# Performance work log

Hardware: AMD Instinct MI355X
Metric: run time of the kernel (lower is better)

The kernel has to match this reference:

```python
import jax, jax.numpy as jnp
import numpy as np

N_NODES = 100000


def _gcn_layer(x, W, b, src, dst, n):
    # PyG GCNConv: x' = D^-1/2 (A+I) D^-1/2 (x W) + b, with self-loops added.
    x = x @ W  # [N, out]
    loop = jnp.arange(n, dtype=src.dtype)
    src_f = jnp.concatenate([src, loop])
    dst_f = jnp.concatenate([dst, loop])
    deg = jax.ops.segment_sum(jnp.ones_like(dst_f, dtype=x.dtype), dst_f, num_segments=n)
    dinv = jnp.where(deg > 0, jax.lax.rsqrt(deg), 0.0)
    norm = dinv[src_f] * dinv[dst_f]  # [E+N]
    msgs = x[src_f] * norm[:, None]   # gather + scale
    out = jax.ops.segment_sum(msgs, dst_f, num_segments=n)
    return out + b


def setup_inputs() -> dict:
    key = jax.random.key(0)
    ks = jax.random.split(key, 16)
    inputFeatures = jax.random.normal(ks[0], (N_NODES, 64), dtype=jnp.float32)
    edge_index = jax.random.randint(ks[1], (2, 1000000), 0, N_NODES, dtype=jnp.int64)

    def lin(k, fan_in, fan_out):
        s = 1.0 / np.sqrt(fan_in)
        return jax.random.uniform(k, (fan_in, fan_out), jnp.float32, -s, s)

    return {
        "inputFeatures": inputFeatures,
        "W1": lin(ks[2], 64, 100), "b1": jnp.zeros((100,), jnp.float32),
        "W2": lin(ks[3], 100, 50), "b2": jnp.zeros((50,), jnp.float32),
        "W3": lin(ks[4], 50, 25), "b3": jnp.zeros((25,), jnp.float32),
        "Wl1": lin(ks[5], 25, 25), "bl1": jnp.zeros((25,), jnp.float32),
        "Wl2": lin(ks[6], 25, 10), "bl2": jnp.zeros((10,), jnp.float32),
        "Wl3": lin(ks[7], 10, 1), "bl3": jnp.zeros((1,), jnp.float32),
        "edge_index": edge_index,
    }


def reference(inputFeatures, W1, b1, W2, b2, W3, b3, Wl1, bl1, Wl2, bl2, Wl3, bl3, edge_index):
    src, dst = edge_index[0], edge_index[1]
    n = inputFeatures.shape[0]
    x = jax.nn.relu(_gcn_layer(inputFeatures, W1, b1, src, dst, n))
    x = jax.nn.relu(_gcn_layer(x, W2, b2, src, dst, n))
    x = jax.nn.relu(_gcn_layer(x, W3, b3, src, dst, n))
    x = jax.nn.relu(x @ Wl1 + bl1)
    x = jax.nn.relu(x @ Wl2 + bl2)
    x = jax.nn.relu(x @ Wl3 + bl3)
    return x  # [N, 1]
```

## Files before the change

### kernel.cpp

```cpp
#include <hip/hip_runtime.h>
#include <hip/hip_fp16.h>
#include <cstdint>

constexpr int BSHIFT = 9;
constexpr int NBUCK  = 256;
constexpr int BUCKET_CAP = 6144;
constexpr int BN = 1 << BSHIFT;
constexpr int NT = 8;

struct alignas(16) H8 { __half2 a, b, c, d; };
struct alignas(8)  H4 { __half2 a, b; };

typedef _Float16 f16x8 __attribute__((ext_vector_type(8)));
typedef float    f32x4 __attribute__((ext_vector_type(4)));

__device__ __forceinline__ float4 add4(float4 a, float4 b) {
    return make_float4(a.x + b.x, a.y + b.y, a.z + b.z, a.w + b.w);
}
__device__ __forceinline__ float4 mul4s(float4 a, float s) {
    return make_float4(a.x * s, a.y * s, a.z * s, a.w * s);
}
__device__ __forceinline__ void acc_h8(float4& A0, float4& A1, const H8 v, float s) {
    float2 f0 = __half22float2(v.a), f1 = __half22float2(v.b);
    float2 f2 = __half22float2(v.c), f3 = __half22float2(v.d);
    A0.x = fmaf(f0.x, s, A0.x); A0.y = fmaf(f0.y, s, A0.y);
    A0.z = fmaf(f1.x, s, A0.z); A0.w = fmaf(f1.y, s, A0.w);
    A1.x = fmaf(f2.x, s, A1.x); A1.y = fmaf(f2.y, s, A1.y);
    A1.z = fmaf(f3.x, s, A1.z); A1.w = fmaf(f3.y, s, A1.w);
}


constexpr int EPT = 16;
__global__ __launch_bounds__(256) void partition_pack(
    const int* __restrict__ src, const int* __restrict__ dst,
    int* __restrict__ bucketCur, int* __restrict__ pairs, int ne, int nEdgeBlocks,
    const float* __restrict__ W1, const float* __restrict__ W2,
    const float* __restrict__ W3,
    __half* __restrict__ P1, __half* __restrict__ P2, __half* __restrict__ P3) {
    if (blockIdx.x == (unsigned)nEdgeBlocks) {
        int t = threadIdx.x;
        for (int i = t; i < 7 * 2 * 64 * 8; i += 256) {
            int j = i & 7, lane = (i >> 3) & 63, f = i >> 9;
            int mt = f >> 1, kf = f & 1;
            int k = kf * 32 + (lane >> 4) * 8 + j;
            int m = mt * 16 + (lane & 15);
            P1[i] = __float2half_rn(m < 100 ? W1[k * 100 + m] : 0.0f);
        }
        for (int i = t; i < 4 * 4 * 64 * 8; i += 256) {
            int j = i & 7, lane = (i >> 3) & 63, f = i >> 9;
            int mt = f >> 2, kf = f & 3;
            int k = kf * 32 + (lane >> 4) * 8 + j;
            int m = mt * 16 + (lane & 15);
            P2[i] = __float2half_rn((k < 100 && m < 50) ? W2[k * 50 + m] : 0.0f);
        }
        for (int i = t; i < 2 * 2 * 64 * 8; i += 256) {
            int j = i & 7, lane = (i >> 3) & 63, f = i >> 9;
            int mt = f >> 1, kf = f & 1;
            int k = kf * 32 + (lane >> 4) * 8 + j;
            int m = mt * 16 + (lane & 15);
            P3[i] = __float2half_rn((k < 50 && m < 25) ? W3[k * 25 + m] : 0.0f);
        }
        return;
    }
    __shared__ int lcnt[NBUCK];
    __shared__ int lbase[NBUCK];
    int base = blockIdx.x * (256 * EPT);
    if (threadIdx.x < NBUCK) lcnt[threadIdx.x] = 0;
    __syncthreads();
    int2 ed[EPT];
    int  rnk[EPT];
#pragma unroll
    for (int j = 0; j < EPT; ++j) {
        int e = base + j * 256 + threadIdx.x;
        if (e < ne) {
            int d = dst[e];
            ed[j] = make_int2(src[e], d);
            rnk[j] = atomicAdd(&lcnt[d >> BSHIFT], 1);
        } else {
            ed[j].y = -1;
        }
    }
    __syncthreads();
    if (threadIdx.x < NBUCK) {
        int c = lcnt[threadIdx.x];
        lbase[threadIdx.x] = c ? atomicAdd(&bucketCur[threadIdx.x], c) : 0;
    }
    __syncthreads();
#pragma unroll
    for (int j = 0; j < EPT; ++j) {
        if (ed[j].y >= 0) {
            int b = ed[j].y >> BSHIFT;
            int p = lbase[b] + rnk[j];
            if (p < BUCKET_CAP)
                pairs[(size_t)b * BUCKET_CAP + p] =
                    (ed[j].x << BSHIFT) | (ed[j].y & (BN - 1));
        }
    }
}

__global__ __launch_bounds__(256) void bucket_csr_scan(
    const int* __restrict__ pairs, const int* __restrict__ bucketCnt,
    int* __restrict__ offs, float* __restrict__ dinv, int* __restrict__ csr,
    int n, int ne, int nbuckets) {
    __shared__ int pos2[BN * NT];
    __shared__ int tmp[256];
    __shared__ int baseS;
    int b = blockIdx.x;
    int t = threadIdx.x;

    int c = (t < (unsigned)nbuckets) ? bucketCnt[t] : 0;
    tmp[t] = c;
    for (int i = t; i < BN * NT; i += 256) pos2[i] = 0;
    __syncthreads();
    for (int off = 1; off < 256; off <<= 1) {
        int v = (t >= (unsigned)off) ? tmp[t - off] : 0;
        __syncthreads();
        tmp[t] += v;
        __syncthreads();
    }
    if (t == 0) {
        baseS = b ? tmp[b - 1] : 0;
        if (b == 0) offs[n] = ne;
    }
    __syncthreads();
    int base = baseS;
    int cnt  = bucketCnt[b];
    const int* pb = pairs + (size_t)b * BUCKET_CAP;
    int nodeLo = b << BSHIFT;

    for (int e = t; e < cnt; e += 256) {
        int p = pb[e];
        atomicAdd(&pos2[(p & (BN - 1)) * NT + (((unsigned)p) >> (BSHIFT + 14))], 1);
    }
    __syncthreads();

    {
        int lo = t * 16;
        int s = 0;
#pragma unroll
        for (int i = 0; i < 16; ++i) { int v = pos2[lo + i]; pos2[lo + i] = s; s += v; }
        tmp[t] = s;
        __syncthreads();
        for (int off = 1; off < 256; off <<= 1) {
            int v = (t >= (unsigned)off) ? tmp[t - off] : 0;
            __syncthreads();
            tmp[t] += v;
            __syncthreads();
        }
        int add = t ? tmp[t - 1] : 0;
#pragma unroll
        for (int i = 0; i < 16; ++i) pos2[lo + i] += add;
    }
    __syncthreads();

    int l0 = 2 * t, l1 = l0 + 1;
    int s0 = pos2[l0 * NT];
    int s1 = pos2[l1 * NT];
    int s2 = (t < 255) ? pos2[(l1 + 1) * NT] : cnt;
    int h0 = s1 - s0, h1 = s2 - s1;
    int g0 = nodeLo + l0, g1 = nodeLo + l1;
    if (g0 < n) { offs[g0] = base + s0; dinv[g0] = rsqrtf((float)(h0 + 1)); }
    if (g1 < n) { offs[g1] = base + s1; dinv[g1] = rsqrtf((float)(h1 + 1)); }
    __syncthreads();

    for (int e = t; e < cnt; e += 256) {
        int p = pb[e];
        int idx = (p & (BN - 1)) * NT + (((unsigned)p) >> (BSHIFT + 14));
        int pos = atomicAdd(&pos2[idx], 1);
        csr[base + pos] = ((unsigned)p) >> BSHIFT;
    }
}

__global__ void cvt_scale_f32_f16(const float* __restrict__ x, const float* __restrict__ dinv,
                                  __half* __restrict__ o, int n4) {
    int i = blockIdx.x * blockDim.x + threadIdx.x;
    if (i < n4) {
        float dv = dinv[i >> 4];
        float4 v = ((const float4*)x)[i];
        H4 h;
        h.a = __floats2half2_rn(v.x * dv, v.y * dv);
        h.b = __floats2half2_rn(v.z * dv, v.w * dv);
        ((H4*)o)[i] = h;
    }
}

constexpr int XSP = 72;
constexpr int HPS = 136;
__global__ __launch_bounds__(256, 4) void agg1gemm12(
    const __half* __restrict__ x, const int* __restrict__ offs,
    const int* __restrict__ csr, const float* __restrict__ dinv,
    const __half* __restrict__ P1, const float* __restrict__ b1,
    const __half* __restrict__ P2, __half* __restrict__ out, int n) {
    __shared__ alignas(16) _Float16 Xs[64 * XSP];
    __shared__ alignas(16) _Float16 Hs[64 * HPS];
    int tid = threadIdx.x, lane = tid & 63, w = tid >> 6;
    int lg = lane >> 4, lr = lane & 15;
    int blockBase = blockIdx.x * 64;

    for (int i = tid; i < 64 * 2; i += 256) {
        f16x8 zz = {};
        *(f16x8*)&Hs[(i >> 1) * HPS + 112 + (i & 1) * 8] = zz;
    }

    int f0 = (lane & 7) * 8;
#pragma unroll
    for (int p = 0; p < 2; ++p) {
        int nl = w * 16 + p * 8 + (lane >> 3);
        int node = blockBase + nl;
        float4 z4 = make_float4(0.f, 0.f, 0.f, 0.f);
        float4 a00 = z4, a01 = z4, a10 = z4, a11 = z4, a20 = z4, a21 = z4, a30 = z4, a31 = z4;
        float dv = 0.0f;
        if (node < n) {
            dv = dinv[node];
            H8 sv = *(const H8*)&x[(size_t)node * 64 + f0];
            acc_h8(a00, a01, sv, 1.0f);
            int e0 = offs[node], e1 = offs[node + 1];
            int e = e0;
            for (; e + 4 <= e1; e += 4) {
                int i0 = csr[e], i1 = csr[e + 1], i2 = csr[e + 2], i3 = csr[e + 3];
                H8 v0 = *(const H8*)&x[(size_t)i0 * 64 + f0];
                H8 v1 = *(const H8*)&x[(size_t)i1 * 64 + f0];
                H8 v2 = *(const H8*)&x[(size_t)i2 * 64 + f0];
                H8 v3 = *(const H8*)&x[(size_t)i3 * 64 + f0];
                acc_h8(a00, a01, v0, 1.0f);
                acc_h8(a10, a11, v1, 1.0f);
                acc_h8(a20, a21, v2, 1.0f);
                acc_h8(a30, a31, v3, 1.0f);
            }
            for (; e < e1; ++e) {
                H8 v = *(const H8*)&x[(size_t)csr[e] * 64 + f0];
                acc_h8(a00, a01, v, 1.0f);
            }
        }
        float4 A0 = add4(add4(a00, a10), add4(a20, a30));
        float4 A1 = add4(add4(a01, a11), add4(a21, a31));
        A0 = mul4s(A0, dv);
        A1 = mul4s(A1, dv);
        H8 h;
        h.a = __floats2half2_rn(A0.x, A0.y);
        h.b = __floats2half2_rn(A0.z, A0.w);
        h.c = __floats2half2_rn(A1.x, A1.y);
        h.d = __floats2half2_rn(A1.z, A1.w);
        *(H8*)&Xs[nl * XSP + f0] = h;
    }
    __syncthreads();

    const f16x8* P1v = (const f16x8*)P1;
    float b1v[7];
#pragma unroll
    for (int mt = 0; mt < 7; ++mt) {
        int m = mt * 16 + lr;
        b1v[mt] = (m < 100) ? b1[m] : 0.0f;
    }
    {
        int rowL = w * 16 + lr;
        f16x8 a0 = *(const f16x8*)&Xs[rowL * XSP + lg * 8];
        f16x8 a1 = *(const f16x8*)&Xs[rowL * XSP + 32 + lg * 8];
        int hbase = w * 16;
#pragma unroll
        for (int mt = 0; mt < 7; ++mt) {
            f16x8 w0 = P1v[(mt * 2 + 0) * 64 + lane];
            f16x8 w1 = P1v[(mt * 2 + 1) * 64 + lane];
            f32x4 acc = {};
            acc = __builtin_amdgcn_mfma_f32_16x16x32_f16(a0, w0, acc, 0, 0, 0);
            acc = __builtin_amdgcn_mfma_f32_16x16x32_f16(a1, w1, acc, 0, 0, 0);
            int col = mt * 16 + lr;
#pragma unroll
            for (int i = 0; i < 4; ++i) {
                int rloc = hbase + lg * 4 + i;
                Hs[rloc * HPS + col] = (_Float16)fmaxf(acc[i] + b1v[mt], 0.0f);
            }
        }
    }
    __syncthreads();

    const f16x8* P2v = (const f16x8*)P2;
#pragma unroll
    for (int mt = 0; mt < 4; ++mt) {
        f16x8 w0 = P2v[(mt * 4 + 0) * 64 + lane];
        f16x8 w1 = P2v[(mt * 4 + 1) * 64 + lane];
        f16x8 w2 = P2v[(mt * 4 + 2) * 64 + lane];
        f16x8 w3 = P2v[(mt * 4 + 3) * 64 + lane];
        int lbase = w * 16;
        const _Float16* hrow = &Hs[(size_t)(lbase + lr) * HPS];
        f16x8 a0 = *(const f16x8*)&hrow[lg * 8];
        f16x8 a1 = *(const f16x8*)&hrow[32 + lg * 8];
        f16x8 a2 = *(const f16x8*)&hrow[64 + lg * 8];
        f16x8 a3 = *(const f16x8*)&hrow[96 + lg * 8];
        f32x4 acc = {};
        acc = __builtin_amdgcn_mfma_f32_16x16x32_f16(a0, w0, acc, 0, 0, 0);
        acc = __builtin_amdgcn_mfma_f32_16x16x32_f16(a1, w1, acc, 0, 0, 0);
        acc = __builtin_amdgcn_mfma_f32_16x16x32_f16(a2, w2, acc, 0, 0, 0);
        acc = __builtin_amdgcn_mfma_f32_16x16x32_f16(a3, w3, acc, 0, 0, 0);
        int col = mt * 16 + lr;
#pragma unroll
        for (int i = 0; i < 4; ++i) {
            int node = blockBase + lbase + lg * 4 + i;
            if (node < n)
                out[(size_t)node * 64 + col] = __float2half_rn(acc[i] * dinv[node]);
        }
    }
}

constexpr int YP = 72;
__global__ __launch_bounds__(256) void agg2g3(
    const __half* __restrict__ s, const int* __restrict__ offs,
    const int* __restrict__ csr, const float* __restrict__ dinv,
    const float* __restrict__ b2, const __half* __restrict__ P3,
    __half* __restrict__ out, int n) {
    __shared__ alignas(16) _Float16 Ys[32 * YP];
    int tid = threadIdx.x, lane = tid & 63, w = tid >> 6;
    int lg = lane >> 4, lr = lane & 15;
    int blockBase = blockIdx.x * 32;

    int nodeL = tid >> 3;
    int f0 = (tid & 7) * 8;
    int node = blockBase + nodeL;
    float v[8] = {0.f, 0.f, 0.f, 0.f, 0.f, 0.f, 0.f, 0.f};
    if (node < n && f0 < 56) {
        float dv = dinv[node];
        float4 z4 = make_float4(0.f, 0.f, 0.f, 0.f);
        float4 a00 = z4, a01 = z4, a10 = z4, a11 = z4, a20 = z4, a21 = z4, a30 = z4, a31 = z4;
        {
            H8 sv = *(const H8*)&s[(size_t)node * 64 + f0];
            acc_h8(a00, a01, sv, 1.0f);
        }
        int e0 = offs[node], e1 = offs[node + 1];
        int e = e0;
        for (; e + 4 <= e1; e += 4) {
            int i0 = csr[e], i1 = csr[e + 1], i2 = csr[e + 2], i3 = csr[e + 3];
            H8 v0 = *(const H8*)&s[(size_t)i0 * 64 + f0];
            H8 v1 = *(const H8*)&s[(size_t)i1 * 64 + f0];
            H8 v2 = *(const H8*)&s[(size_t)i2 * 64 + f0];
            H8 v3 = *(const H8*)&s[(size_t)i3 * 64 + f0];
            acc_h8(a00, a01, v0, 1.0f);
            acc_h8(a10, a11, v1, 1.0f);
            acc_h8(a20, a21, v2, 1.0f);
            acc_h8(a30, a31, v3, 1.0f);
        }
        for (; e < e1; ++e) {
            H8 vv = *(const H8*)&s[(size_t)csr[e] * 64 + f0];
            acc_h8(a00, a01, vv, 1.0f);
        }
        float4 A0 = add4(add4(a00, a10), add4(a20, a30));
        float4 A1 = add4(add4(a01, a11), add4(a21, a31));
        float vr[8] = {A0.x, A0.y, A0.z, A0.w, A1.x, A1.y, A1.z, A1.w};
#pragma unroll
        for (int i = 0; i < 8; ++i)
            v[i] = (f0 + i < 50) ? fmaxf(dv * vr[i] + b2[f0 + i], 0.0f) : 0.0f;
    }
    {
        H8 h;
        h.a = __floats2half2_rn(v[0], v[1]);
        h.b = __floats2half2_rn(v[2], v[3]);
        h.c = __floats2half2_rn(v[4], v[5]);
        h.d = __floats2half2_rn(v[6], v[7]);
        *(H8*)&Ys[nodeL * YP + f0] = h;
    }
    __syncthreads();

    int rt = w >> 1, mt = w & 1;
    const f16x8* P3v = (const f16x8*)P3;
    f16x8 w0 = P3v[(mt * 2 + 0) * 64 + lane];
    f16x8 w1 = P3v[(mt * 2 + 1) * 64 + lane];
    int rowL = rt * 16 + lr;
    f16x8 a0 = *(const f16x8*)&Ys[rowL * YP + lg * 8];
    f16x8 a1 = *(const f16x8*)&Ys[rowL * YP + 32 + lg * 8];
    f32x4 acc = {};
    acc = __builtin_amdgcn_mfma_f32_16x16x32_f16(a0, w0, acc, 0, 0, 0);
    acc = __builtin_amdgcn_mfma_f32_16x16x32_f16(a1, w1, acc, 0, 0, 0);
    int col = mt * 16 + lr;
#pragma unroll
    for (int i = 0; i < 4; ++i) {
        int nd = blockBase + rt * 16 + lg * 4 + i;
        if (nd < n)
            out[(size_t)nd * 32 + col] = __float2half_rn(acc[i] * dinv[nd]);
    }
}

__global__ __launch_bounds__(256) void agg3_mlp_h(
    const __half* __restrict__ s, const int* __restrict__ offs,
    const int* __restrict__ csr, const float* __restrict__ dinv,
    const float* __restrict__ bg,
    const float* __restrict__ Wl1, const float* __restrict__ bl1,
    const float* __restrict__ Wl2, const float* __restrict__ bl2,
    const float* __restrict__ Wl3, const float* __restrict__ bl3,
    float* __restrict__ out, int n) {
    constexpr int LPN = 4;
    __shared__ float W1s[625], W2s[250], W3s[10], b1s[25], b2s[10];
    __shared__ float accs[64 * 26];
    __shared__ float b3s;

    for (int i = threadIdx.x; i < 625; i += 256) W1s[i] = Wl1[i];
    for (int i = threadIdx.x; i < 250; i += 256) W2s[i] = Wl2[i];
    if (threadIdx.x < 10) { W3s[threadIdx.x] = Wl3[threadIdx.x]; b2s[threadIdx.x] = bl2[threadIdx.x]; }
    if (threadIdx.x < 25) b1s[threadIdx.x] = bl1[threadIdx.x];
    if (threadIdx.x == 0) b3s = bl3[0];

    int lane = threadIdx.x % LPN;
    int nl   = threadIdx.x / LPN;
    int node = blockIdx.x * 64 + nl;
    int f0 = lane * 8;

    if (node < n && f0 < 25) {
        float dv = dinv[node];
        float4 z4 = make_float4(0.f, 0.f, 0.f, 0.f);
        float4 a00 = z4, a01 = z4, a10 = z4, a11 = z4, a20 = z4, a21 = z4, a30 = z4, a31 = z4;
        {
            H8 sv = *(const H8*)&s[(size_t)node * 32 + f0];
            acc_h8(a00, a01, sv, 1.0f);
        }
        int e0 = offs[node], e1 = offs[node + 1];
        int e = e0;
        for (; e + 4 <= e1; e += 4) {
            int i0 = csr[e], i1 = csr[e + 1], i2 = csr[e + 2], i3 = csr[e + 3];
            H8 v0 = *(const H8*)&s[(size_t)i0 * 32 + f0];
            H8 v1 = *(const H8*)&s[(size_t)i1 * 32 + f0];
            H8 v2 = *(const H8*)&s[(size_t)i2 * 32 + f0];
            H8 v3 = *(const H8*)&s[(size_t)i3 * 32 + f0];
            acc_h8(a00, a01, v0, 1.0f);
            acc_h8(a10, a11, v1, 1.0f);
            acc_h8(a20, a21, v2, 1.0f);
            acc_h8(a30, a31, v3, 1.0f);
        }
        for (; e < e1; ++e) {
            H8 v = *(const H8*)&s[(size_t)csr[e] * 32 + f0];
            acc_h8(a00, a01, v, 1.0f);
        }
        float4 A0 = add4(add4(a00, a10), add4(a20, a30));
        float4 A1 = add4(add4(a01, a11), add4(a21, a31));
        float v[8] = {A0.x, A0.y, A0.z, A0.w, A1.x, A1.y, A1.z, A1.w};
#pragma unroll
        for (int i = 0; i < 8; ++i)
            if (f0 + i < 25)
                accs[nl * 26 + f0 + i] = fmaxf(dv * v[i] + bg[f0 + i], 0.0f);
    }
    __syncthreads();

    if (threadIdx.x < 64) {
        int nd = blockIdx.x * 64 + threadIdx.x;
        if (nd < n) {
            const float* xr = &accs[threadIdx.x * 26];
            float h1[25];
#pragma unroll
            for (int m = 0; m < 25; ++m) {
                float a = b1s[m];
#pragma unroll
                for (int k = 0; k < 25; ++k) a = fmaf(xr[k], W1s[k * 25 + m], a);
                h1[m] = fmaxf(a, 0.0f);
            }
            float h2[10];
#pragma unroll
            for (int m = 0; m < 10; ++m) {
                float a = b2s[m];
#pragma unroll
                for (int k = 0; k < 25; ++k) a = fmaf(h1[k], W2s[k * 10 + m], a);
                h2[m] = fmaxf(a, 0.0f);
            }
            float a = b3s;
#pragma unroll
            for (int k = 0; k < 10; ++k) a = fmaf(h2[k], W3s[k], a);
            out[nd] = fmaxf(a, 0.0f);
        }
    }
}


extern "C" void kernel_launch(void* const* d_in, const int* in_sizes, int n_in,
                              void* d_out, int out_size, void* d_ws, size_t ws_size,
                              hipStream_t stream) {
    const float* x0  = (const float*)d_in[0];
    const float* W1  = (const float*)d_in[1];
    const float* b1  = (const float*)d_in[2];
    const float* W2  = (const float*)d_in[3];
    const float* b2  = (const float*)d_in[4];
    const float* W3  = (const float*)d_in[5];
    const float* b3  = (const float*)d_in[6];
    const float* Wl1 = (const float*)d_in[7];
    const float* bl1 = (const float*)d_in[8];
    const float* Wl2 = (const float*)d_in[9];
    const float* bl2 = (const float*)d_in[10];
    const float* Wl3 = (const float*)d_in[11];
    const float* bl3 = (const float*)d_in[12];
    const int*   edge = (const int*)d_in[13];

    int n  = in_sizes[0] / 64;
    int ne = in_sizes[13] / 2;
    const int* esrc = edge;
    const int* edst = edge + ne;

    char* ws = (char*)d_ws;
    auto alloc = [&](size_t bytes) {
        char* p = ws;
        ws += (bytes + 255) & ~(size_t)255;
        return p;
    };
    int*    offs       = (int*)alloc((size_t)(n + 1) * 4);
    int*    bucketCur  = (int*)alloc(NBUCK * 4);
    int*    csr        = (int*)alloc((size_t)ne * 4);
    float*  dinv       = (float*)alloc((size_t)n * 4);
    __half* x0h        = (__half*)alloc((size_t)n * 64 * 2);
    __half* bufDh      = (__half*)alloc((size_t)n * 64 * 2);
    __half* bufCh      = (__half*)alloc((size_t)n * 32 * 2);
    __half* P1         = (__half*)alloc(7 * 2 * 64 * 8 * 2);
    __half* P2         = (__half*)alloc(4 * 4 * 64 * 8 * 2);
    __half* P3         = (__half*)alloc(2 * 2 * 64 * 8 * 2);
    int*    pairs = (int*)bufDh;
    (void)ws_size; (void)n_in; (void)out_size;

    int nbuckets = (n + (1 << BSHIFT) - 1) >> BSHIFT;
    int nchunk   = (ne + 256 * EPT - 1) / (256 * EPT);

    hipMemsetAsync(bucketCur, 0, NBUCK * 4, stream);
    partition_pack<<<nchunk + 1, 256, 0, stream>>>(
        esrc, edst, bucketCur, pairs, ne, nchunk, W1, W2, W3, P1, P2, P3);
    bucket_csr_scan<<<nbuckets, 256, 0, stream>>>(
        pairs, bucketCur, offs, dinv, csr, n, ne, nbuckets);

    cvt_scale_f32_f16<<<(n * 16 + 255) / 256, 256, 0, stream>>>(x0, dinv, x0h, n * 16);

    agg1gemm12<<<(n + 63) / 64, 256, 0, stream>>>(
        x0h, offs, csr, dinv, P1, b1, P2, bufDh, n);

    agg2g3<<<(n + 31) / 32, 256, 0, stream>>>(
        bufDh, offs, csr, dinv, b2, P3, bufCh, n);

    agg3_mlp_h<<<(n + 63) / 64, 256, 0, stream>>>(
        bufCh, offs, csr, dinv, b3, Wl1, bl1, Wl2, bl2, Wl3, bl3, (float*)d_out, n);
}
```

Measured before the change: 232.8 us.

## Simplify CSR bucket scan and stage MFMA outputs in LDS for vector stores

The CSR build drops the 8-way sub-histogram per node that ordered edges by source high bits. It now uses a single per-node histogram, one scan, and a cursor array, which cuts LDS size, atomics and scan work, but the order of edges within a row is no longer deterministic. The two MFMA-based kernels now write their scaled outputs into shared memory first and then emit 16-byte coalesced global stores instead of scattered 2-byte stores. The A fragments and dinv values are hoisted out of the column loop. This adds extra barriers and an LDS round trip.

```diff
diff --git a/kernel.cpp b/kernel.cpp
--- a/kernel.cpp
+++ b/kernel.cpp
@@ -6,7 +6,6 @@
 constexpr int NBUCK  = 256;
 constexpr int BUCKET_CAP = 6144;
 constexpr int BN = 1 << BSHIFT;
-constexpr int NT = 8;
 
 struct alignas(16) H8 { __half2 a, b, c, d; };
 struct alignas(8)  H4 { __half2 a, b; };
@@ -102,7 +101,8 @@
     const int* __restrict__ pairs, const int* __restrict__ bucketCnt,
     int* __restrict__ offs, float* __restrict__ dinv, int* __restrict__ csr,
     int n, int ne, int nbuckets) {
-    __shared__ int pos2[BN * NT];
+    __shared__ int hist[BN];
+    __shared__ int cur[BN];
     __shared__ int tmp[256];
     __shared__ int baseS;
     int b = blockIdx.x;
@@ -110,7 +110,6 @@
 
     int c = (t < (unsigned)nbuckets) ? bucketCnt[t] : 0;
     tmp[t] = c;
-    for (int i = t; i < BN * NT; i += 256) pos2[i] = 0;
     __syncthreads();
     for (int off = 1; off < 256; off <<= 1) {
         int v = (t >= (unsigned)off) ? tmp[t - off] : 0;
@@ -128,45 +127,35 @@
     const int* pb = pairs + (size_t)b * BUCKET_CAP;
     int nodeLo = b << BSHIFT;
 
+    hist[t] = 0;
+    hist[t + 256] = 0;
+    __syncthreads();
+    for (int e = t; e < cnt; e += 256)
+        atomicAdd(&hist[pb[e] & (BN - 1)], 1);
+    __syncthreads();
+
+    int l0 = 2 * t, l1 = l0 + 1;
+    int h0 = hist[l0], h1 = hist[l1];
+    tmp[t] = h0 + h1;
+    __syncthreads();
+    for (int off = 1; off < 256; off <<= 1) {
+        int v = (t >= (unsigned)off) ? tmp[t - off] : 0;
+        __syncthreads();
+        tmp[t] += v;
+        __syncthreads();
+    }
+    int e0 = tmp[t] - (h0 + h1);
+    int e1 = e0 + h0;
+    int g0 = nodeLo + l0, g1 = nodeLo + l1;
+    if (g0 < n) { offs[g0] = base + e0; dinv[g0] = rsqrtf((float)(h0 + 1)); }
+    if (g1 < n) { offs[g1] = base + e1; dinv[g1] = rsqrtf((float)(h1 + 1)); }
+    cur[l0] = e0;
+    cur[l1] = e1;
+    __syncthreads();
+
     for (int e = t; e < cnt; e += 256) {
         int p = pb[e];
-        atomicAdd(&pos2[(p & (BN - 1)) * NT + (((unsigned)p) >> (BSHIFT + 14))], 1);
-    }
-    __syncthreads();
-
-    {
-        int lo = t * 16;
-        int s = 0;
-#pragma unroll
-        for (int i = 0; i < 16; ++i) { int v = pos2[lo + i]; pos2[lo + i] = s; s += v; }
-        tmp[t] = s;
-        __syncthreads();
-        for (int off = 1; off < 256; off <<= 1) {
-            int v = (t >= (unsigned)off) ? tmp[t - off] : 0;
-            __syncthreads();
-            tmp[t] += v;
-            __syncthreads();
-        }
-        int add = t ? tmp[t - 1] : 0;
-#pragma unroll
-        for (int i = 0; i < 16; ++i) pos2[lo + i] += add;
-    }
-    __syncthreads();
-
-    int l0 = 2 * t, l1 = l0 + 1;
-    int s0 = pos2[l0 * NT];
-    int s1 = pos2[l1 * NT];
-    int s2 = (t < 255) ? pos2[(l1 + 1) * NT] : cnt;
-    int h0 = s1 - s0, h1 = s2 - s1;
-    int g0 = nodeLo + l0, g1 = nodeLo + l1;
-    if (g0 < n) { offs[g0] = base + s0; dinv[g0] = rsqrtf((float)(h0 + 1)); }
-    if (g1 < n) { offs[g1] = base + s1; dinv[g1] = rsqrtf((float)(h1 + 1)); }
-    __syncthreads();
-
-    for (int e = t; e < cnt; e += 256) {
-        int p = pb[e];
-        int idx = (p & (BN - 1)) * NT + (((unsigned)p) >> (BSHIFT + 14));
-        int pos = atomicAdd(&pos2[idx], 1);
+        int pos = atomicAdd(&cur[p & (BN - 1)], 1);
         csr[base + pos] = ((unsigned)p) >> BSHIFT;
     }
 }
@@ -275,18 +264,24 @@
     __syncthreads();
 
     const f16x8* P2v = (const f16x8*)P2;
+    int lbase = w * 16;
+    const _Float16* hrow = &Hs[(size_t)(lbase + lr) * HPS];
+    f16x8 a0 = *(const f16x8*)&hrow[lg * 8];
+    f16x8 a1 = *(const f16x8*)&hrow[32 + lg * 8];
+    f16x8 a2 = *(const f16x8*)&hrow[64 + lg * 8];
+    f16x8 a3 = *(const f16x8*)&hrow[96 + lg * 8];
+    float dvq[4];
+#pragma unroll
+    for (int i = 0; i < 4; ++i) {
+        int node = blockBase + lbase + lg * 4 + i;
+        dvq[i] = (node < n) ? dinv[node] : 0.0f;
+    }
 #pragma unroll
     for (int mt = 0; mt < 4; ++mt) {
         f16x8 w0 = P2v[(mt * 4 + 0) * 64 + lane];
         f16x8 w1 = P2v[(mt * 4 + 1) * 64 + lane];
         f16x8 w2 = P2v[(mt * 4 + 2) * 64 + lane];
         f16x8 w3 = P2v[(mt * 4 + 3) * 64 + lane];
-        int lbase = w * 16;
-        const _Float16* hrow = &Hs[(size_t)(lbase + lr) * HPS];
-        f16x8 a0 = *(const f16x8*)&hrow[lg * 8];
-        f16x8 a1 = *(const f16x8*)&hrow[32 + lg * 8];
-        f16x8 a2 = *(const f16x8*)&hrow[64 + lg * 8];
-        f16x8 a3 = *(const f16x8*)&hrow[96 + lg * 8];
         f32x4 acc = {};
         acc = __builtin_amdgcn_mfma_f32_16x16x32_f16(a0, w0, acc, 0, 0, 0);
         acc = __builtin_amdgcn_mfma_f32_16x16x32_f16(a1, w1, acc, 0, 0, 0);
@@ -294,11 +289,16 @@
         acc = __builtin_amdgcn_mfma_f32_16x16x32_f16(a3, w3, acc, 0, 0, 0);
         int col = mt * 16 + lr;
 #pragma unroll
-        for (int i = 0; i < 4; ++i) {
-            int node = blockBase + lbase + lg * 4 + i;
-            if (node < n)
-                out[(size_t)node * 64 + col] = __float2half_rn(acc[i] * dinv[node]);
-        }
+        for (int i = 0; i < 4; ++i)
+            Xs[(lbase + lg * 4 + i) * XSP + col] = (_Float16)(acc[i] * dvq[i]);
+    }
+    __syncthreads();
+
+    for (int i = tid; i < 64 * 8; i += 256) {
+        int r = i >> 3, cc = (i & 7) * 8;
+        int node = blockBase + r;
+        if (node < n)
+            *(H8*)&out[(size_t)node * 64 + cc] = *(const H8*)&Xs[r * XSP + cc];
     }
 }
 
@@ -369,12 +369,22 @@
     f32x4 acc = {};
     acc = __builtin_amdgcn_mfma_f32_16x16x32_f16(a0, w0, acc, 0, 0, 0);
     acc = __builtin_amdgcn_mfma_f32_16x16x32_f16(a1, w1, acc, 0, 0, 0);
+    __syncthreads();
     int col = mt * 16 + lr;
 #pragma unroll
     for (int i = 0; i < 4; ++i) {
-        int nd = blockBase + rt * 16 + lg * 4 + i;
+        int rl = rt * 16 + lg * 4 + i;
+        int nd = blockBase + rl;
+        float dv = (nd < n) ? dinv[nd] : 0.0f;
+        Ys[rl * YP + col] = (_Float16)(acc[i] * dv);
+    }
+    __syncthreads();
+
+    if (tid < 128) {
+        int r = tid >> 2, cc = (tid & 3) * 8;
+        int nd = blockBase + r;
         if (nd < n)
-            out[(size_t)nd * 32 + col] = __float2half_rn(acc[i] * dinv[nd]);
+            *(H8*)&out[(size_t)nd * 32 + cc] = *(const H8*)&Ys[r * YP + cc];
     }
 }
 
```

Measured after the change: 228.3 us, median of 2. About the same (-1.9%).
